# Optimization experiments

Measured on AMD Instinct MI355X. Metric: run time of the kernel, lower is better.

The kernel has to match this reference:

```python
import jax, jax.numpy as jnp
import numpy as np

EMBED_DIM = 400
HEAD_SIZE = 64


def setup_inputs() -> dict:
    key = jax.random.key(0)
    k1, k2, k3, k4 = jax.random.split(key, 4)
    B, T, C = 8, 2048, EMBED_DIM
    x = jax.random.normal(k1, (B, T, C), dtype=jnp.float32)
    # Linear(embed_dim, head_size, bias=False) weights, stored as [C, H] for x @ W
    s = 1.0 / np.sqrt(C)
    Wq = jax.random.uniform(k2, (C, HEAD_SIZE), dtype=jnp.float32, minval=-s, maxval=s)
    Wk = jax.random.uniform(k3, (C, HEAD_SIZE), dtype=jnp.float32, minval=-s, maxval=s)
    Wv = jax.random.uniform(k4, (C, HEAD_SIZE), dtype=jnp.float32, minval=-s, maxval=s)
    return {"x": x, "Wq": Wq, "Wk": Wk, "Wv": Wv}


def reference(x, Wq, Wk, Wv):
    B, T, C = x.shape
    q = x @ Wq  # [B,T,H]
    k = x @ Wk  # [B,T,H]
    v = x @ Wv  # [B,T,H]
    scale = 1.0 / jnp.sqrt(jnp.asarray(q.shape[-1], q.dtype))
    scores = jnp.einsum('bth,bsh->bts', q, k) * scale  # [B,T,T]
    causal = jnp.tril(jnp.ones((T, T), dtype=bool))
    scores = jnp.where(causal, scores, jnp.asarray(-jnp.inf, scores.dtype))
    attn = jax.nn.softmax(scores, axis=-1)
    out = jnp.einsum('bts,bsh->bth', attn, v)  # [B,T,H]
    return out
```

## Files before the change

kernel.cpp:

```cpp
#include <hip/hip_runtime.h>
#include <math.h>

#define B_SZ   8
#define T_SEQ  2048
#define C_DIM  400
#define H_DIM  64
#define NROWS  (B_SZ * T_SEQ)
#define QT_TILES (T_SEQ / 64)
#define KPAD   416
#define LDSTR  424
#define NCH    8
#define TPC    4

typedef short s8v  __attribute__((ext_vector_type(8)));
typedef float f32x4 __attribute__((ext_vector_type(4)));

__device__ __forceinline__ unsigned short f2bf(float f) {
    unsigned int u = __float_as_uint(f);
    u = (u + 0x7FFFu + ((u >> 16) & 1u)) >> 16;
    return (unsigned short)u;
}

__device__ __forceinline__ float bf2f(unsigned short u) {
    return __uint_as_float((unsigned)u << 16);
}

__device__ __forceinline__ unsigned cvtpk_bf16(float lo, float hi) {
    unsigned r;
    asm("v_cvt_pk_bf16_f32 %0, %1, %2" : "=v"(r) : "v"(lo), "v"(hi));
    return r;
}

__global__ __launch_bounds__(256) void wprep_kernel(
    const float* __restrict__ Wq, const float* __restrict__ Wk,
    const float* __restrict__ Wv, unsigned short* __restrict__ Wt)
{
    int idx = blockIdx.x * 256 + threadIdx.x;
    if (idx >= 3 * H_DIM * KPAD) return;
    int m = idx / (H_DIM * KPAD);
    int r = idx - m * (H_DIM * KPAD);
    int h = r / KPAD;
    int k = r - h * KPAD;
    const float* W = (m == 0) ? Wq : (m == 1) ? Wk : Wv;
    float v = (k < C_DIM) ? W[k * H_DIM + h] : 0.0f;
    if (m == 0) v *= 0.125f * 1.44269504088896f;
    Wt[idx] = f2bf(v);
}

__global__ __launch_bounds__(256) void proj_kernel(
    const float* __restrict__ x, const unsigned short* __restrict__ Wt,
    unsigned short* __restrict__ Qb, unsigned short* __restrict__ Kb,
    unsigned short* __restrict__ Vt)
{
    __shared__ unsigned short xl[16 * LDSTR];
    const int tid = threadIdx.x;
    const int tile = blockIdx.x;

    const float4* __restrict__ x4 = (const float4*)x;
    for (int idx = tid; idx < 16 * 104; idx += 256) {
        int row = idx / 104, c4 = idx - row * 104;
        ushort4 w;
        if (c4 < 100) {
            float4 v = x4[(size_t)(tile * 16 + row) * 100 + c4];
            w.x = f2bf(v.x); w.y = f2bf(v.y); w.z = f2bf(v.z); w.w = f2bf(v.w);
        } else { w.x = w.y = w.z = w.w = 0; }
        *(ushort4*)&xl[row * LDSTR + c4 * 4] = w;
    }
    __syncthreads();

    const int w = tid >> 6, l = tid & 63;
    const int lr = l & 15, g = l >> 4;

    f32x4 acc[3];
    acc[0] = (f32x4)0.f; acc[1] = (f32x4)0.f; acc[2] = (f32x4)0.f;

    for (int ks = 0; ks < KPAD / 32; ++ks) {
        s8v a = *(const s8v*)&xl[lr * LDSTR + ks * 32 + g * 8];
#pragma unroll
        for (int fl = 0; fl < 3; ++fl) {
            int f = w * 3 + fl;
            int col = (f & 3) * 16 + lr;
            const s8v b = *(const s8v*)&Wt[((size_t)(f >> 2) * H_DIM + col) * KPAD
                                           + ks * 32 + g * 8];
            acc[fl] = __builtin_amdgcn_mfma_f32_16x16x32_bf16(a, b, acc[fl], 0, 0, 0);
        }
    }

#pragma unroll
    for (int fl = 0; fl < 3; ++fl) {
        int f = w * 3 + fl;
        int m = f >> 2, col = (f & 3) * 16 + lr;
#pragma unroll
        for (int r = 0; r < 4; ++r) {
            int row_g = tile * 16 + g * 4 + r;
            unsigned short bv = f2bf(acc[fl][r]);
            if (m == 0)      Qb[(size_t)row_g * H_DIM + col] = bv;
            else if (m == 1) Kb[(size_t)row_g * H_DIM + col] = bv;
            else {
                int b = row_g >> 11, t = row_g & 2047;
                Vt[((size_t)b * H_DIM + col) * T_SEQ + t] = bv;
            }
        }
    }
}

__global__ __launch_bounds__(256) void attn_kernel(
    const unsigned short* __restrict__ Qb, const unsigned short* __restrict__ Kb,
    const unsigned short* __restrict__ Vt,
    unsigned short* __restrict__ Opart, float* __restrict__ lpart)
{
    const int c  = blockIdx.x;
    const int qt = blockIdx.y;
    const int b  = blockIdx.z;
    if (c * TPC > qt) return;
    const int kt0 = c * TPC;
    const int kend = min(kt0 + (TPC - 1), qt);

    __shared__ char smem[2][16384];

    const int tid = threadIdx.x;
    const int w = tid >> 6, l = tid & 63;
    const int lr = l & 15, g = l >> 4;
    const int q0 = qt * 64 + w * 16;

    const int r0 = tid >> 3;
    const int ch = tid & 7;
    const int swz = (ch * 16) ^ ((r0 & 7) << 4);
    const char* const Kg = (const char*)(Kb + (size_t)b * T_SEQ * H_DIM);
    const char* const Vg = (const char*)(Vt + (size_t)b * H_DIM * T_SEQ);

    uint4 kA, kB, vA, vB;
    auto LD = [&](int kt) {
        kA = *(const uint4*)(Kg + (size_t)(kt * 64 + r0     ) * 128 + ch * 16);
        kB = *(const uint4*)(Kg + (size_t)(kt * 64 + r0 + 32) * 128 + ch * 16);
        vA = *(const uint4*)(Vg + (size_t)(r0     ) * 4096 + kt * 128 + ch * 16);
        vB = *(const uint4*)(Vg + (size_t)(r0 + 32) * 4096 + kt * 128 + ch * 16);
    };
    auto ST = [&](int buf) {
        char* Kl = smem[buf];
        char* Vl = smem[buf] + 8192;
        *(uint4*)(Kl + r0 * 128 + swz)        = kA;
        *(uint4*)(Kl + (r0 + 32) * 128 + swz) = kB;
        *(uint4*)(Vl + r0 * 128 + swz)        = vA;
        *(uint4*)(Vl + (r0 + 32) * 128 + swz) = vB;
    };

    s8v aq[2];
#pragma unroll
    for (int s = 0; s < 2; ++s)
        aq[s] = *(const s8v*)&Qb[((size_t)b * T_SEQ + q0 + lr) * H_DIM + s * 32 + g * 8];

    f32x4 acc[4];
#pragma unroll
    for (int f = 0; f < 4; ++f) acc[f] = (f32x4)0.f;
    float lsum = 0.f;

    LD(kt0); ST(0);
    if (kt0 < kend) LD(kt0 + 1);
    __syncthreads();
    int cur = 0;

    for (int kt = kt0; kt <= kend; ++kt) {
        char* const Kl = smem[cur];
        char* const Vl = smem[cur] + 8192;

        f32x4 sacc[4];
#pragma unroll
        for (int f = 0; f < 4; ++f) sacc[f] = (f32x4)0.f;
        __builtin_amdgcn_s_setprio(1);
#pragma unroll
        for (int f = 0; f < 4; ++f)
#pragma unroll
            for (int s = 0; s < 2; ++s) {
                const s8v ak = *(const s8v*)(Kl + (f * 16 + lr) * 128
                                             + (((s * 4 + g) * 16) ^ ((lr & 7) << 4)));
                sacc[f] = __builtin_amdgcn_mfma_f32_16x16x32_bf16(ak, aq[s], sacc[f], 0, 0, 0);
            }
        __builtin_amdgcn_s_setprio(0);

        float p[4][4];
        const bool diag = (kt == qt);
        const int q_my = q0 + lr;
#pragma unroll
        for (int f = 0; f < 4; ++f)
#pragma unroll
            for (int r = 0; r < 4; ++r) {
                float pv = __builtin_amdgcn_exp2f(sacc[f][r]);
                if (diag && (kt * 64 + f * 16 + g * 4 + r) > q_my) pv = 0.0f;
                p[f][r] = pv;
                lsum += pv;
            }

        s8v ap[2];
#pragma unroll
        for (int s = 0; s < 2; ++s) {
            unsigned Fa = cvtpk_bf16(p[2 * s][0],     p[2 * s][1]);
            unsigned Fb = cvtpk_bf16(p[2 * s][2],     p[2 * s][3]);
            unsigned Ga = cvtpk_bf16(p[2 * s + 1][0], p[2 * s + 1][1]);
            unsigned Gb = cvtpk_bf16(p[2 * s + 1][2], p[2 * s + 1][3]);
            asm("v_permlane32_swap_b32 %0, %1" : "+v"(Fa), "+v"(Ga));
            asm("v_permlane16_swap_b32 %0, %1" : "+v"(Fa), "+v"(Ga));
            asm("v_permlane32_swap_b32 %0, %1" : "+v"(Fb), "+v"(Gb));
            asm("v_permlane16_swap_b32 %0, %1" : "+v"(Fb), "+v"(Gb));
            unsigned wds[4] = { Fa, Fb, Ga, Gb };
            ap[s] = *(const s8v*)wds;
        }

        __builtin_amdgcn_s_setprio(1);
#pragma unroll
        for (int f = 0; f < 4; ++f)
#pragma unroll
            for (int s = 0; s < 2; ++s) {
                const s8v bv = *(const s8v*)(Vl + (f * 16 + lr) * 128
                                             + (((s * 4 + g) * 16) ^ ((lr & 7) << 4)));
                acc[f] = __builtin_amdgcn_mfma_f32_16x16x32_bf16(ap[s], bv, acc[f], 0, 0, 0);
            }
        __builtin_amdgcn_s_setprio(0);

        if (kt < kend) {
            ST(cur ^ 1);
            if (kt + 1 < kend) LD(kt + 2);
            __syncthreads();
            cur ^= 1;
        }
    }

    lsum += __shfl_xor(lsum, 16, 64);
    lsum += __shfl_xor(lsum, 32, 64);

    const size_t pb = ((size_t)(b * QT_TILES + qt) * NCH + c);
    unsigned short* const Op = Opart + pb * 4096;
#pragma unroll
    for (int f = 0; f < 4; ++f)
#pragma unroll
        for (int r = 0; r < 4; ++r)
            Op[(w * 16 + g * 4 + r) * 64 + f * 16 + lr] = f2bf(acc[f][r]);
    if (l < 16)
        lpart[pb * 64 + w * 16 + l] = lsum;
}

__global__ __launch_bounds__(256) void combine_kernel(
    const unsigned short* __restrict__ Opart, const float* __restrict__ lpart,
    float* __restrict__ out)
{
    const int idx = blockIdx.x * 256 + threadIdx.x;
    const int row = idx >> 4, h4 = idx & 15;
    const int b = row >> 11, t = row & 2047;
    const int qt = t >> 6, r = t & 63;
    const int nch = (qt >> 2) + 1;

    float4 os = make_float4(0.f, 0.f, 0.f, 0.f);
    float ls = 0.f;
    const size_t base = (size_t)(b * QT_TILES + qt) * NCH;
    for (int cc = 0; cc < nch; ++cc) {
        ushort4 v = *(const ushort4*)&Opart[(base + cc) * 4096 + r * 64 + h4 * 4];
        os.x += bf2f(v.x); os.y += bf2f(v.y); os.z += bf2f(v.z); os.w += bf2f(v.w);
        ls += lpart[(base + cc) * 64 + r];
    }
    float inv = 1.0f / ls;
    ((float4*)out)[idx] = make_float4(os.x * inv, os.y * inv, os.z * inv, os.w * inv);
}

extern "C" void kernel_launch(void* const* d_in, const int* in_sizes, int n_in,
                              void* d_out, int out_size, void* d_ws, size_t ws_size,
                              hipStream_t stream)
{
    const float* x  = (const float*)d_in[0];
    const float* Wq = (const float*)d_in[1];
    const float* Wk = (const float*)d_in[2];
    const float* Wv = (const float*)d_in[3];
    float* out = (float*)d_out;

    char* ws = (char*)d_ws;
    unsigned short* Wt = (unsigned short*)(ws);
    unsigned short* Qb = (unsigned short*)(ws + 163840);
    unsigned short* Kb = (unsigned short*)(ws + 163840 + 2097152);
    unsigned short* Vt = (unsigned short*)(ws + 163840 + 2 * 2097152);
    unsigned short* Opart = (unsigned short*)(ws + 163840 + 3 * 2097152);
    float* lpart = (float*)(ws + 163840 + 3 * 2097152 + 16777216);

    wprep_kernel<<<(3 * H_DIM * KPAD + 255) / 256, 256, 0, stream>>>(Wq, Wk, Wv, Wt);
    proj_kernel<<<NROWS / 16, 256, 0, stream>>>(x, Wt, Qb, Kb, Vt);
    attn_kernel<<<dim3(NCH, QT_TILES, B_SZ), 256, 0, stream>>>(Qb, Kb, Vt, Opart, lpart);
    combine_kernel<<<(NROWS * H_DIM / 4) / 256, 256, 0, stream>>>(Opart, lpart, out);
}
```

Before: 51.26 us.

## Double projection rows per block and pre-swizzle weights into MFMA fragment order

The projection kernel now processes 32 rows per block instead of 16, so each weight fragment load feeds two MFMAs. The weight prep kernel writes weights in per-lane fragment order, which turns each B load into one contiguous 16-byte access per lane. The attention kernel splits the causal masking into a diagonal branch and an unmasked branch and tree-sums the row sums. The cost is twice the LDS per projection block and half as many projection blocks, which lowers parallelism in that stage.

```diff
diff --git a/kernel.cpp b/kernel.cpp
--- a/kernel.cpp
+++ b/kernel.cpp
@@ -7,13 +7,14 @@
 #define H_DIM  64
 #define NROWS  (B_SZ * T_SEQ)
 #define QT_TILES (T_SEQ / 64)
-#define KPAD   416
 #define LDSTR  424
 #define NCH    8
 #define TPC    4
+#define NKS    13
 
 typedef short s8v  __attribute__((ext_vector_type(8)));
 typedef float f32x4 __attribute__((ext_vector_type(4)));
+typedef unsigned u32x4 __attribute__((ext_vector_type(4)));
 
 __device__ __forceinline__ unsigned short f2bf(float f) {
     unsigned int u = __float_as_uint(f);
@@ -33,56 +34,63 @@
 
 __global__ __launch_bounds__(256) void wprep_kernel(
     const float* __restrict__ Wq, const float* __restrict__ Wk,
-    const float* __restrict__ Wv, unsigned short* __restrict__ Wt)
+    const float* __restrict__ Wv, unsigned short* __restrict__ WtP)
 {
     int idx = blockIdx.x * 256 + threadIdx.x;
-    if (idx >= 3 * H_DIM * KPAD) return;
-    int m = idx / (H_DIM * KPAD);
-    int r = idx - m * (H_DIM * KPAD);
-    int h = r / KPAD;
-    int k = r - h * KPAD;
+    int j    = idx & 7;
+    int lane = (idx >> 3) & 63;
+    int fks  = idx >> 9;
+    int f    = fks / NKS;
+    int ks   = fks - f * NKS;
+    int m    = f >> 2;
+    int col  = (f & 3) * 16 + (lane & 15);
+    int k    = ks * 32 + (lane >> 4) * 8 + j;
     const float* W = (m == 0) ? Wq : (m == 1) ? Wk : Wv;
-    float v = (k < C_DIM) ? W[k * H_DIM + h] : 0.0f;
+    float v = (k < C_DIM) ? W[k * H_DIM + col] : 0.0f;
     if (m == 0) v *= 0.125f * 1.44269504088896f;
-    Wt[idx] = f2bf(v);
+    WtP[idx] = f2bf(v);
 }
 
 __global__ __launch_bounds__(256) void proj_kernel(
-    const float* __restrict__ x, const unsigned short* __restrict__ Wt,
+    const float* __restrict__ x, const unsigned short* __restrict__ WtP,
     unsigned short* __restrict__ Qb, unsigned short* __restrict__ Kb,
     unsigned short* __restrict__ Vt)
 {
-    __shared__ unsigned short xl[16 * LDSTR];
+    __shared__ unsigned short xl[32 * LDSTR];
     const int tid = threadIdx.x;
     const int tile = blockIdx.x;
 
     const float4* __restrict__ x4 = (const float4*)x;
-    for (int idx = tid; idx < 16 * 104; idx += 256) {
+    for (int idx = tid; idx < 32 * 104; idx += 256) {
         int row = idx / 104, c4 = idx - row * 104;
-        ushort4 w;
+        ushort4 wv;
         if (c4 < 100) {
-            float4 v = x4[(size_t)(tile * 16 + row) * 100 + c4];
-            w.x = f2bf(v.x); w.y = f2bf(v.y); w.z = f2bf(v.z); w.w = f2bf(v.w);
-        } else { w.x = w.y = w.z = w.w = 0; }
-        *(ushort4*)&xl[row * LDSTR + c4 * 4] = w;
+            float4 v = x4[(size_t)(tile * 32 + row) * 100 + c4];
+            wv.x = f2bf(v.x); wv.y = f2bf(v.y); wv.z = f2bf(v.z); wv.w = f2bf(v.w);
+        } else { wv.x = wv.y = wv.z = wv.w = 0; }
+        *(ushort4*)&xl[row * LDSTR + c4 * 4] = wv;
     }
     __syncthreads();
 
     const int w = tid >> 6, l = tid & 63;
     const int lr = l & 15, g = l >> 4;
 
-    f32x4 acc[3];
-    acc[0] = (f32x4)0.f; acc[1] = (f32x4)0.f; acc[2] = (f32x4)0.f;
-
-    for (int ks = 0; ks < KPAD / 32; ++ks) {
-        s8v a = *(const s8v*)&xl[lr * LDSTR + ks * 32 + g * 8];
+    f32x4 acc[3][2];
+#pragma unroll
+    for (int fl = 0; fl < 3; ++fl)
+#pragma unroll
+        for (int rg = 0; rg < 2; ++rg) acc[fl][rg] = (f32x4)0.f;
+
+    const char* const Wp = (const char*)WtP;
+    for (int ks = 0; ks < NKS; ++ks) {
+        s8v a0 = *(const s8v*)&xl[lr        * LDSTR + ks * 32 + g * 8];
+        s8v a1 = *(const s8v*)&xl[(16 + lr) * LDSTR + ks * 32 + g * 8];
 #pragma unroll
         for (int fl = 0; fl < 3; ++fl) {
             int f = w * 3 + fl;
-            int col = (f & 3) * 16 + lr;
-            const s8v b = *(const s8v*)&Wt[((size_t)(f >> 2) * H_DIM + col) * KPAD
-                                           + ks * 32 + g * 8];
-            acc[fl] = __builtin_amdgcn_mfma_f32_16x16x32_bf16(a, b, acc[fl], 0, 0, 0);
+            const s8v b = *(const s8v*)(Wp + ((f * NKS + ks) << 10) + (l << 4));
+            acc[fl][0] = __builtin_amdgcn_mfma_f32_16x16x32_bf16(a0, b, acc[fl][0], 0, 0, 0);
+            acc[fl][1] = __builtin_amdgcn_mfma_f32_16x16x32_bf16(a1, b, acc[fl][1], 0, 0, 0);
         }
     }
 
@@ -91,16 +99,18 @@
         int f = w * 3 + fl;
         int m = f >> 2, col = (f & 3) * 16 + lr;
 #pragma unroll
-        for (int r = 0; r < 4; ++r) {
-            int row_g = tile * 16 + g * 4 + r;
-            unsigned short bv = f2bf(acc[fl][r]);
-            if (m == 0)      Qb[(size_t)row_g * H_DIM + col] = bv;
-            else if (m == 1) Kb[(size_t)row_g * H_DIM + col] = bv;
-            else {
-                int b = row_g >> 11, t = row_g & 2047;
-                Vt[((size_t)b * H_DIM + col) * T_SEQ + t] = bv;
+        for (int rg = 0; rg < 2; ++rg)
+#pragma unroll
+            for (int r = 0; r < 4; ++r) {
+                int row_g = tile * 32 + rg * 16 + g * 4 + r;
+                unsigned short bv = f2bf(acc[fl][rg][r]);
+                if (m == 0)      Qb[(size_t)row_g * H_DIM + col] = bv;
+                else if (m == 1) Kb[(size_t)row_g * H_DIM + col] = bv;
+                else {
+                    int b = row_g >> 11, t = row_g & 2047;
+                    Vt[((size_t)b * H_DIM + col) * T_SEQ + t] = bv;
+                }
             }
-        }
     }
 }
 
@@ -179,17 +189,25 @@
         __builtin_amdgcn_s_setprio(0);
 
         float p[4][4];
-        const bool diag = (kt == qt);
-        const int q_my = q0 + lr;
+        if (kt == qt) {
+            const int q_my = q0 + lr;
+#pragma unroll
+            for (int f = 0; f < 4; ++f)
+#pragma unroll
+                for (int r = 0; r < 4; ++r) {
+                    float pv = __builtin_amdgcn_exp2f(sacc[f][r]);
+                    p[f][r] = ((kt * 64 + f * 16 + g * 4 + r) > q_my) ? 0.0f : pv;
+                }
+        } else {
+#pragma unroll
+            for (int f = 0; f < 4; ++f)
+#pragma unroll
+                for (int r = 0; r < 4; ++r)
+                    p[f][r] = __builtin_amdgcn_exp2f(sacc[f][r]);
+        }
 #pragma unroll
         for (int f = 0; f < 4; ++f)
-#pragma unroll
-            for (int r = 0; r < 4; ++r) {
-                float pv = __builtin_amdgcn_exp2f(sacc[f][r]);
-                if (diag && (kt * 64 + f * 16 + g * 4 + r) > q_my) pv = 0.0f;
-                p[f][r] = pv;
-                lsum += pv;
-            }
+            lsum += (p[f][0] + p[f][1]) + (p[f][2] + p[f][3]);
 
         s8v ap[2];
 #pragma unroll
@@ -202,8 +220,8 @@
             asm("v_permlane16_swap_b32 %0, %1" : "+v"(Fa), "+v"(Ga));
             asm("v_permlane32_swap_b32 %0, %1" : "+v"(Fb), "+v"(Gb));
             asm("v_permlane16_swap_b32 %0, %1" : "+v"(Fb), "+v"(Gb));
-            unsigned wds[4] = { Fa, Fb, Ga, Gb };
-            ap[s] = *(const s8v*)wds;
+            u32x4 wv; wv.x = Fa; wv.y = Fb; wv.z = Ga; wv.w = Gb;
+            ap[s] = __builtin_bit_cast(s8v, wv);
         }
 
         __builtin_amdgcn_s_setprio(1);
@@ -272,15 +290,15 @@
     float* out = (float*)d_out;
 
     char* ws = (char*)d_ws;
-    unsigned short* Wt = (unsigned short*)(ws);
+    unsigned short* WtP = (unsigned short*)(ws);
     unsigned short* Qb = (unsigned short*)(ws + 163840);
     unsigned short* Kb = (unsigned short*)(ws + 163840 + 2097152);
     unsigned short* Vt = (unsigned short*)(ws + 163840 + 2 * 2097152);
     unsigned short* Opart = (unsigned short*)(ws + 163840 + 3 * 2097152);
     float* lpart = (float*)(ws + 163840 + 3 * 2097152 + 16777216);
 
-    wprep_kernel<<<(3 * H_DIM * KPAD + 255) / 256, 256, 0, stream>>>(Wq, Wk, Wv, Wt);
-    proj_kernel<<<NROWS / 16, 256, 0, stream>>>(x, Wt, Qb, Kb, Vt);
+    wprep_kernel<<<(12 * NKS * 512) / 256, 256, 0, stream>>>(Wq, Wk, Wv, WtP);
+    proj_kernel<<<NROWS / 32, 256, 0, stream>>>(x, WtP, Qb, Kb, Vt);
     attn_kernel<<<dim3(NCH, QT_TILES, B_SZ), 256, 0, stream>>>(Qb, Kb, Vt, Opart, lpart);
     combine_kernel<<<(NROWS * H_DIM / 4) / 256, 256, 0, stream>>>(Opart, lpart, out);
 }
```

Result: faster. 43.77 us (-14.6%).
